# Optimization experiments

Measured on AMD Instinct MI355X. Metric: run time of the kernel, lower is better.

Reference implementation:

```python
import jax, jax.numpy as jnp
import numpy as np
import math

HEAD = 4

def _neighbors3x3(t):
    # t: [b, g, d, h, w] -> [b, g, d, 9, h, w], zero-padded 3x3 neighborhoods
    b, g, d, h, w = t.shape
    tp = jnp.pad(t, ((0, 0), (0, 0), (0, 0), (1, 1), (1, 1)))
    # torch.nn.Unfold(kernel_size=3) ordering: kernel positions row-major (dy, dx)
    patches = [tp[:, :, :, dy:dy + h, dx:dx + w] for dy in range(3) for dx in range(3)]
    return jnp.stack(patches, axis=3)


def setup_inputs() -> dict:
    key = jax.random.key(0)
    k1, k2 = jax.random.split(key)
    x = jax.random.normal(k1, (8, 128, 96, 96), dtype=jnp.float32)
    # 1x1 conv weight, no bias: [out=3*out_features, in=in_features]
    W_trans = jax.random.normal(k2, (384, 128), dtype=jnp.float32) * 0.05
    return {"x": x, "W_trans": W_trans}


def reference(x, W_trans):
    b, cin, h, w = x.shape
    # 1x1 conv == channel GEMM
    t = jnp.einsum('bchw,oc->bohw', x, W_trans)  # [b, 3*C, h, w]
    q, k, v = jnp.split(t, 3, axis=1)            # each [b, C, h, w]
    C = q.shape[1]
    d = C // HEAD
    q = q.reshape(b, HEAD, d, h, w)
    k = k.reshape(b, HEAD, d, h, w)
    v = v.reshape(b, HEAD, d, h, w)
    kn = _neighbors3x3(k)  # [b, g, d, 9, h, w]
    vn = _neighbors3x3(v)  # [b, g, d, 9, h, w]
    # att[b,g,n,h,w] = <q[b,g,:,h,w], kn[b,g,:,n,h,w]> / sqrt(d)
    att = jnp.einsum('bgdhw,bgdnhw->bgnhw', q, kn) / math.sqrt(d)
    att = jax.nn.softmax(att, axis=2)
    # dropout p=0.4 is identity in eval mode
    out = jnp.einsum('bgnhw,bgdnhw->bgdhw', att, vn)  # [b, g, d, h, w]
    return out.reshape(b, C, h, w)
```

## Files before the change

### kernel.cpp

```cpp
#include <hip/hip_runtime.h>

#define NB    8
#define CIN   128
#define HDIM  96
#define WDIM  96
#define HW    9216
#define TW    16
#define TH    4
#define HXW   18
#define NHX   108
#define NHXP  112
#define NMT   7
#define KV_REC 272
#define Q_REC  144
#define KV_BYTES (NHXP * KV_REC)
#define Q_BYTES  (NHXP * Q_REC)
#define LDS_U4   ((KV_BYTES + Q_BYTES) / 16)

typedef __bf16 bf16x8 __attribute__((ext_vector_type(8)));
typedef float  f32x4  __attribute__((ext_vector_type(4)));

__device__ __forceinline__ unsigned f2bf(float f) {
  unsigned u = __float_as_uint(f);
  return (u + 0x7fffu + ((u >> 16) & 1u)) >> 16;
}
__device__ __forceinline__ unsigned pack2(float a, float b) {
  return f2bf(a) | (f2bf(b) << 16);
}
__device__ __forceinline__ float bflo(unsigned u) { return __uint_as_float(u << 16); }
__device__ __forceinline__ float bfhi(unsigned u) { return __uint_as_float(u & 0xffff0000u); }

__global__ __launch_bounds__(256) void wpack_kernel(const float* __restrict__ W,
                                                    uint4* __restrict__ Wf) {
  const int u = blockIdx.x * 256 + threadIdx.x;
  const int lane = u & 63, kb = (u >> 6) & 3, ot = u >> 8;
  const int o = ot * 16 + (lane & 15);
  const int c0 = kb * 32 + (lane >> 4) * 8;
  const float4* w = (const float4*)(W + (size_t)o * CIN + c0);
  float4 w0 = w[0], w1 = w[1];
  uint4 r;
  r.x = pack2(w0.x, w0.y); r.y = pack2(w0.z, w0.w);
  r.z = pack2(w1.x, w1.y); r.w = pack2(w1.z, w1.w);
  Wf[u] = r;
}

__global__ __launch_bounds__(256, 3) void fused_kernel(
    const float* __restrict__ x, const uint4* __restrict__ Wf,
    float* __restrict__ out) {
  __shared__ uint4 lds4[LDS_U4];
  uint4* xs4  = lds4;
  char* kvb   = (char*)lds4;
  char* qb    = (char*)lds4 + KV_BYTES;

  const int t  = threadIdx.x;
  const int w0 = blockIdx.x * TW, h0 = blockIdx.y * TH;
  const int b  = blockIdx.z;
  const int lane = t & 63, wv = t >> 6;

#pragma unroll
  for (int i = 0; i < 7; ++i) {
    const int id  = i * 256 + t;
    const int oct = id / NHXP;
    const int hx  = id - oct * NHXP;
    const int r   = hx / HXW;
    const int ww  = hx - r * HXW;
    const int h = h0 - 1 + r, w = w0 - 1 + ww;
    const bool valid = (hx < NHX) && ((unsigned)h < HDIM) && ((unsigned)w < WDIM);
    float f[8];
    if (valid) {
      const float* xb = x + ((size_t)(b * CIN + oct * 8)) * HW + h * WDIM + w;
#pragma unroll
      for (int jv = 0; jv < 8; ++jv) f[jv] = xb[(size_t)jv * HW];
    } else {
#pragma unroll
      for (int jv = 0; jv < 8; ++jv) f[jv] = 0.f;
    }
    uint4 rv;
    rv.x = pack2(f[0], f[1]); rv.y = pack2(f[2], f[3]);
    rv.z = pack2(f[4], f[5]); rv.w = pack2(f[6], f[7]);
    xs4[((hx >> 4) * 4 + (oct >> 2)) * 64 + (oct & 3) * 16 + (hx & 15)] = rv;
  }
  __syncthreads();

  uint4 bfr[NMT][4];
#pragma unroll
  for (int mt = 0; mt < NMT; ++mt)
#pragma unroll
    for (int kb = 0; kb < 4; ++kb)
      bfr[mt][kb] = xs4[(mt * 4 + kb) * 64 + lane];
  __syncthreads();

  const int colp = lane & 15, quad = lane >> 4;
  const int px = t >> 2, g2 = (t >> 1) & 1, dh = t & 1;
  const int pr = px >> 4, pw = px & 15;
  const int hx0 = (pr + 1) * HXW + pw + 1;
  const int hoff = g2 * 64 + dh * 32;

#pragma unroll 1
  for (int hp = 0; hp < 2; ++hp) {
#pragma unroll
    for (int jj = 0; jj < 3; ++jj) {
      const int j = wv * 3 + jj;
      const int which = j >> 2, jo = j & 3;
      const int ot = which * 8 + hp * 4 + jo;
      uint4 af[4];
#pragma unroll
      for (int kb = 0; kb < 4; ++kb) af[kb] = Wf[(ot * 4 + kb) * 64 + lane];
      const int lc = jo * 16 + quad * 4;
      char* base; int rec;
      if (which == 0) { base = qb + lc * 2; rec = Q_REC; }
      else { base = kvb + (which - 1) * 128 + lc * 2; rec = KV_REC; }
#pragma unroll
      for (int mt = 0; mt < NMT; ++mt) {
        f32x4 acc = {0.f, 0.f, 0.f, 0.f};
#pragma unroll
        for (int kb = 0; kb < 4; ++kb)
          acc = __builtin_amdgcn_mfma_f32_16x16x32_bf16(
              *(bf16x8*)&af[kb], *(bf16x8*)&bfr[mt][kb], acc, 0, 0, 0);
        uint2 st;
        st.x = pack2(acc[0], acc[1]);
        st.y = pack2(acc[2], acc[3]);
        *(uint2*)(base + (mt * 16 + colp) * rec) = st;
      }
    }
    __syncthreads();

    {
      float q[16];
      {
        const uint4* qp = (const uint4*)(qb + hx0 * Q_REC + hoff);
        uint4 u0 = qp[0], u1 = qp[1];
        q[0]=bflo(u0.x);  q[1]=bfhi(u0.x);  q[2]=bflo(u0.y);  q[3]=bfhi(u0.y);
        q[4]=bflo(u0.z);  q[5]=bfhi(u0.z);  q[6]=bflo(u0.w);  q[7]=bfhi(u0.w);
        q[8]=bflo(u1.x);  q[9]=bfhi(u1.x);  q[10]=bflo(u1.y); q[11]=bfhi(u1.y);
        q[12]=bflo(u1.z); q[13]=bfhi(u1.z); q[14]=bflo(u1.w); q[15]=bfhi(u1.w);
      }

      float att[9];
#pragma unroll
      for (int nn = 0; nn < 9; ++nn) {
        const int hxn = hx0 + (nn / 3 - 1) * HXW + (nn % 3 - 1);
        const uint4* kp = (const uint4*)(kvb + hxn * KV_REC + hoff);
        uint4 k0 = kp[0], k1 = kp[1];
        float dot = 0.f;
        dot = fmaf(q[0],  bflo(k0.x), dot); dot = fmaf(q[1],  bfhi(k0.x), dot);
        dot = fmaf(q[2],  bflo(k0.y), dot); dot = fmaf(q[3],  bfhi(k0.y), dot);
        dot = fmaf(q[4],  bflo(k0.z), dot); dot = fmaf(q[5],  bfhi(k0.z), dot);
        dot = fmaf(q[6],  bflo(k0.w), dot); dot = fmaf(q[7],  bfhi(k0.w), dot);
        dot = fmaf(q[8],  bflo(k1.x), dot); dot = fmaf(q[9],  bfhi(k1.x), dot);
        dot = fmaf(q[10], bflo(k1.y), dot); dot = fmaf(q[11], bfhi(k1.y), dot);
        dot = fmaf(q[12], bflo(k1.z), dot); dot = fmaf(q[13], bfhi(k1.z), dot);
        dot = fmaf(q[14], bflo(k1.w), dot); dot = fmaf(q[15], bfhi(k1.w), dot);
        dot += __shfl_xor(dot, 1);
        att[nn] = dot * 0.17677669529663687f;
      }

      float m = att[0];
#pragma unroll
      for (int nn = 1; nn < 9; ++nn) m = fmaxf(m, att[nn]);
      float s = 0.f;
#pragma unroll
      for (int nn = 0; nn < 9; ++nn) { att[nn] = __expf(att[nn] - m); s += att[nn]; }
      const float inv = 1.0f / s;

      float acc[16];
#pragma unroll
      for (int i = 0; i < 16; ++i) acc[i] = 0.f;
#pragma unroll
      for (int nn = 0; nn < 9; ++nn) {
        const int hxn = hx0 + (nn / 3 - 1) * HXW + (nn % 3 - 1);
        const uint4* vp = (const uint4*)(kvb + hxn * KV_REC + 128 + hoff);
        uint4 v0 = vp[0], v1 = vp[1];
        const float wn = att[nn] * inv;
        acc[0]  = fmaf(wn, bflo(v0.x), acc[0]);  acc[1]  = fmaf(wn, bfhi(v0.x), acc[1]);
        acc[2]  = fmaf(wn, bflo(v0.y), acc[2]);  acc[3]  = fmaf(wn, bfhi(v0.y), acc[3]);
        acc[4]  = fmaf(wn, bflo(v0.z), acc[4]);  acc[5]  = fmaf(wn, bfhi(v0.z), acc[5]);
        acc[6]  = fmaf(wn, bflo(v0.w), acc[6]);  acc[7]  = fmaf(wn, bfhi(v0.w), acc[7]);
        acc[8]  = fmaf(wn, bflo(v1.x), acc[8]);  acc[9]  = fmaf(wn, bfhi(v1.x), acc[9]);
        acc[10] = fmaf(wn, bflo(v1.y), acc[10]); acc[11] = fmaf(wn, bfhi(v1.y), acc[11]);
        acc[12] = fmaf(wn, bflo(v1.z), acc[12]); acc[13] = fmaf(wn, bfhi(v1.z), acc[13]);
        acc[14] = fmaf(wn, bflo(v1.w), acc[14]); acc[15] = fmaf(wn, bfhi(v1.w), acc[15]);
      }

      float* ob = out + ((size_t)(b * CIN + hp * 64 + g2 * 32 + dh * 16)) * HW
                  + (h0 + pr) * WDIM + w0 + pw;
#pragma unroll
      for (int i = 0; i < 16; ++i) ob[(size_t)i * HW] = acc[i];
    }
    if (hp == 0) __syncthreads();
  }
}

extern "C" void kernel_launch(void* const* d_in, const int* in_sizes, int n_in,
                              void* d_out, int out_size, void* d_ws, size_t ws_size,
                              hipStream_t stream) {
  (void)in_sizes; (void)n_in; (void)out_size; (void)ws_size;
  const float* x = (const float*)d_in[0];
  const float* W = (const float*)d_in[1];
  float* out = (float*)d_out;
  uint4* Wf = (uint4*)d_ws;

  wpack_kernel<<<24, 256, 0, stream>>>(W, Wf);
  fused_kernel<<<dim3(WDIM / TW, HDIM / TH, NB), 256, 0, stream>>>(x, Wf, out);
}
```

Baseline: 135.9 us.

## Split GEMM M-tiles across waves and shrink Q LDS buffer for occupancy

Instead of each wave holding all 7 halo M-tiles of x in registers and computing 3 output tiles, waves now split the M-tiles (4 or 3 per wave) and each computes 6 output tiles, cutting the B-fragment register footprint. Q is stored only for the 64 interior pixels rather than the full halo, shrinking LDS. Launch bounds rise from 3 to 4 blocks per SIMD group to exploit the lower register and LDS use. The cost is more weight-fragment loads per wave, uneven work between waves, and extra index math with a branch in the Q store path.

```diff
diff --git a/kernel.cpp b/kernel.cpp
--- a/kernel.cpp
+++ b/kernel.cpp
@@ -14,7 +14,7 @@
 #define KV_REC 272
 #define Q_REC  144
 #define KV_BYTES (NHXP * KV_REC)
-#define Q_BYTES  (NHXP * Q_REC)
+#define Q_BYTES  (64 * Q_REC)
 #define LDS_U4   ((KV_BYTES + Q_BYTES) / 16)
 
 typedef __bf16 bf16x8 __attribute__((ext_vector_type(8)));
@@ -44,7 +44,7 @@
   Wf[u] = r;
 }
 
-__global__ __launch_bounds__(256, 3) void fused_kernel(
+__global__ __launch_bounds__(256, 4) void fused_kernel(
     const float* __restrict__ x, const uint4* __restrict__ Wf,
     float* __restrict__ out) {
   __shared__ uint4 lds4[LDS_U4];
@@ -82,12 +82,15 @@
   }
   __syncthreads();
 
-  uint4 bfr[NMT][4];
-#pragma unroll
-  for (int mt = 0; mt < NMT; ++mt)
-#pragma unroll
-    for (int kb = 0; kb < 4; ++kb)
-      bfr[mt][kb] = xs4[(mt * 4 + kb) * 64 + lane];
+  const int mt0 = (wv & 2) ? 4 : 0;
+  const int nmt = (wv & 2) ? 3 : 4;
+  uint4 bfr[4][4];
+#pragma unroll
+  for (int m = 0; m < 4; ++m)
+    if (m < nmt)
+#pragma unroll
+      for (int kb = 0; kb < 4; ++kb)
+        bfr[m][kb] = xs4[((mt0 + m) * 4 + kb) * 64 + lane];
   __syncthreads();
 
   const int colp = lane & 15, quad = lane >> 4;
@@ -95,32 +98,42 @@
   const int pr = px >> 4, pw = px & 15;
   const int hx0 = (pr + 1) * HXW + pw + 1;
   const int hoff = g2 * 64 + dh * 32;
+  const int j0 = (wv & 1) * 6;
 
 #pragma unroll 1
   for (int hp = 0; hp < 2; ++hp) {
 #pragma unroll
-    for (int jj = 0; jj < 3; ++jj) {
-      const int j = wv * 3 + jj;
+    for (int jj = 0; jj < 6; ++jj) {
+      const int j = j0 + jj;
       const int which = j >> 2, jo = j & 3;
       const int ot = which * 8 + hp * 4 + jo;
       uint4 af[4];
 #pragma unroll
       for (int kb = 0; kb < 4; ++kb) af[kb] = Wf[(ot * 4 + kb) * 64 + lane];
       const int lc = jo * 16 + quad * 4;
-      char* base; int rec;
-      if (which == 0) { base = qb + lc * 2; rec = Q_REC; }
-      else { base = kvb + (which - 1) * 128 + lc * 2; rec = KV_REC; }
-#pragma unroll
-      for (int mt = 0; mt < NMT; ++mt) {
-        f32x4 acc = {0.f, 0.f, 0.f, 0.f};
-#pragma unroll
-        for (int kb = 0; kb < 4; ++kb)
-          acc = __builtin_amdgcn_mfma_f32_16x16x32_bf16(
-              *(bf16x8*)&af[kb], *(bf16x8*)&bfr[mt][kb], acc, 0, 0, 0);
-        uint2 st;
-        st.x = pack2(acc[0], acc[1]);
-        st.y = pack2(acc[2], acc[3]);
-        *(uint2*)(base + (mt * 16 + colp) * rec) = st;
+#pragma unroll
+      for (int m = 0; m < 4; ++m) {
+        if (m < nmt) {
+          const int mt = mt0 + m;
+          f32x4 acc = {0.f, 0.f, 0.f, 0.f};
+#pragma unroll
+          for (int kb = 0; kb < 4; ++kb)
+            acc = __builtin_amdgcn_mfma_f32_16x16x32_bf16(
+                *(bf16x8*)&af[kb], *(bf16x8*)&bfr[m][kb], acc, 0, 0, 0);
+          uint2 st;
+          st.x = pack2(acc[0], acc[1]);
+          st.y = pack2(acc[2], acc[3]);
+          const int hx = mt * 16 + colp;
+          if (which == 0) {
+            const int r = hx / HXW, c = hx - r * HXW;
+            if (r >= 1 && r <= TH && c >= 1 && c <= TW) {
+              const int pi = (r - 1) * TW + (c - 1);
+              *(uint2*)(qb + pi * Q_REC + lc * 2) = st;
+            }
+          } else {
+            *(uint2*)(kvb + hx * KV_REC + (which - 1) * 128 + lc * 2) = st;
+          }
+        }
       }
     }
     __syncthreads();
@@ -128,7 +141,7 @@
     {
       float q[16];
       {
-        const uint4* qp = (const uint4*)(qb + hx0 * Q_REC + hoff);
+        const uint4* qp = (const uint4*)(qb + px * Q_REC + hoff);
         uint4 u0 = qp[0], u1 = qp[1];
         q[0]=bflo(u0.x);  q[1]=bfhi(u0.x);  q[2]=bflo(u0.y);  q[3]=bfhi(u0.y);
         q[4]=bflo(u0.z);  q[5]=bfhi(u0.z);  q[6]=bflo(u0.w);  q[7]=bfhi(u0.w);
```

Result: slower. 146.2 us (+7.6%).
